# Kernel optimization log

Measured on AMD Instinct MI355X. Metric: run time of the kernel, lower is better.

## Reference

```python
import jax, jax.numpy as jnp
import numpy as np

B, N, W, D, K = 128, 256, 64, 128, 20
EPS_BN = 1e-5   # BatchNorm eps (eval mode, running stats = (0, 1))
ALPHA = 0.7     # cosine vs temporal-correlation mixing weight
SLOPE = 0.2     # LeakyReLU negative slope in attention


def setup_inputs() -> dict:
    key = jax.random.key(0)
    ks = jax.random.split(key, 10)
    return {
        "data": jax.random.normal(ks[0], (B, N, W), jnp.float32),
        "org_edge_index": jax.random.randint(ks[1], (2, 4), 0, N),  # unused by forward
        "emb_weight": jax.random.normal(ks[2], (N, D), jnp.float32) * 0.1,
        "lin_W": jax.random.normal(ks[3], (W, D), jnp.float32) / np.sqrt(W),
        "att_i": jax.random.normal(ks[4], (D,), jnp.float32) * 0.1,
        "att_j": jax.random.normal(ks[5], (D,), jnp.float32) * 0.1,
        "att_em_i": jax.random.normal(ks[6], (D,), jnp.float32) * 0.1,
        "att_em_j": jax.random.normal(ks[7], (D,), jnp.float32) * 0.1,
        "gnn_bias": jnp.zeros((D,), jnp.float32),
        "bn1_gamma": jnp.ones((D,), jnp.float32),
        "bn1_beta": jnp.zeros((D,), jnp.float32),
        "bn2_gamma": jnp.ones((D,), jnp.float32),
        "bn2_beta": jnp.zeros((D,), jnp.float32),
        "out_W": jax.random.normal(ks[8], (D, 1), jnp.float32) / np.sqrt(D),
        "out_b": jnp.zeros((1,), jnp.float32),
    }


def _gdn_forward(data, emb_weight, lin_W, att_i, att_j, att_em_i, att_em_j,
                 gnn_bias, bn1_gamma, bn1_beta, bn2_gamma, bn2_beta, out_W, out_b):
    B_, N_, W_ = data.shape
    data = jax.lax.stop_gradient(data)  # torch: x = data.clone().detach()
    x = data.reshape(B_ * N_, W_)

    # ---- dynamic graph build (embedding is detached here in the original) ----
    wts = jax.lax.stop_gradient(emb_weight)                      # [N, D]
    nrm = jnp.linalg.norm(wts, axis=-1)
    cos = (wts @ wts.T) / (jnp.outer(nrm, nrm) + 1e-8)
    xr = jnp.transpose(data, (1, 0, 2)).reshape(N_, -1)          # [N, B*W]
    xc = xr - xr.mean(axis=1, keepdims=True)
    cov = xc @ xc.T
    std = jnp.sqrt(jnp.diagonal(cov) + 1e-8)
    corr = cov / (jnp.outer(std, std) + 1e-8)
    sim = ALPHA * cos + (1.0 - ALPHA) * corr
    topk_idx = jax.lax.top_k(sim, K)[1]                          # [N, K]; diag==1.0 so self edge included

    # gated edges: source j = topk neighbor, target i = row node; batched with node offsets.
    gated_j = topk_idx.reshape(-1)                               # [N*K]
    gated_i = jnp.repeat(jnp.arange(N_), K)                      # [N*K]
    offs = jnp.arange(B_) * N_
    src = (gated_j[:, None] + offs[None, :]).reshape(-1)         # [N*K*B]
    dst = (gated_i[:, None] + offs[None, :]).reshape(-1)

    # ---- GAT-style attention (GraphLayer, heads=1, concat=False) ----
    xl = x @ lin_W                                               # [B*N, D]
    emb_all = jnp.tile(emb_weight, (B_, 1))                      # [B*N, D]
    # per-node scores (equivalent to cat((x, emb)) . cat((att, att_em)))
    s_i = xl @ att_i + emb_all @ att_em_i
    s_j = xl @ att_j + emb_all @ att_em_j
    alpha = s_i[dst] + s_j[src]                                  # [E]
    alpha = jnp.where(alpha > 0, alpha, SLOPE * alpha)           # leaky_relu
    nseg = B_ * N_
    amax = jax.ops.segment_max(alpha, dst, num_segments=nseg)
    ex = jnp.exp(alpha - amax[dst])
    denom = jax.ops.segment_sum(ex, dst, num_segments=nseg)
    attw = ex / denom[dst]                                       # softmax over each node's in-edges
    out = jax.ops.segment_sum(xl[src] * attw[:, None], dst, num_segments=nseg)
    out = out + gnn_bias

    # GNNLayer: BatchNorm1d (eval: running stats (0,1)) + ReLU
    out = jax.nn.relu(out / jnp.sqrt(1.0 + EPS_BN) * bn1_gamma + bn1_beta)

    # ---- readout ----
    h = out.reshape(B_, N_, -1) * emb_weight[None]               # [B, N, D]
    h = jax.nn.relu(h / jnp.sqrt(1.0 + EPS_BN) * bn2_gamma + bn2_beta)  # bn_outlayer_in (eval)
    # dropout(0.2) is identity in eval mode
    y = h @ out_W + out_b                                        # OutLayer (layer_num=1): Linear(D, 1)
    return y.reshape(-1, N_)                                     # [B, N]


def reference(data, org_edge_index, emb_weight, lin_W, att_i, att_j, att_em_i, att_em_j,
              gnn_bias, bn1_gamma, bn1_beta, bn2_gamma, bn2_beta, out_W, out_b):
    # org_edge_index is accepted but unused, exactly as in the torch forward.
    return _gdn_forward(data, emb_weight, lin_W, att_i, att_j, att_em_i, att_em_j,
                        gnn_bias, bn1_gamma, bn1_beta, bn2_gamma, bn2_beta, out_W, out_b)
```

## Files before the change

### kernel.cpp

```cpp
#include <hip/hip_runtime.h>
#include <math.h>

#define BB 128
#define NN 256
#define WW 64
#define DD 128
#define KK 20
#define LL (BB*WW)
#define NPAIR (NN*(NN+1)/2)

__global__ __launch_bounds__(256) void k_covpre(const float* __restrict__ data,
                                                const float* __restrict__ emb,
                                                const float* __restrict__ att_em_i,
                                                const float* __restrict__ att_em_j,
                                                float* __restrict__ covp,
                                                double* __restrict__ mean,
                                                float* __restrict__ eemi,
                                                float* __restrict__ eemj,
                                                double* __restrict__ nrm2,
                                                int split, int bpc) {
    const int t = threadIdx.x;
    const int ncov = 20 * split;

    if ((int)blockIdx.x >= ncov) {
        const int pb = blockIdx.x - ncov;
        const int lane = t & 63, wid = t >> 6;
        if (pb < NN) {
            int n = pb;
            double s = 0.0;
            for (int c = 0; c < LL / 256; ++c) {
                int l = t + c * 256;
                int b = l >> 6, w = l & 63;
                s += (double)data[(b * NN + n) * WW + w];
            }
            for (int off = 32; off; off >>= 1) s += __shfl_down(s, off);
            __shared__ double redm[4];
            if (lane == 0) redm[wid] = s;
            __syncthreads();
            if (t == 0) mean[n] = (redm[0] + redm[1] + redm[2] + redm[3]) / (double)LL;
        } else {
            int n = (pb - NN) * 2 + (t >> 7);
            int d = t & 127;
            float e = emb[n * DD + d];
            float pi = e * att_em_i[d];
            float pj = e * att_em_j[d];
            double pn = (double)e * (double)e;
            for (int off = 32; off; off >>= 1) {
                pi += __shfl_down(pi, off);
                pj += __shfl_down(pj, off);
                pn += __shfl_down(pn, off);
            }
            __shared__ float ri[4], rj[4];
            __shared__ double rn[4];
            if (lane == 0) { ri[wid] = pi; rj[wid] = pj; rn[wid] = pn; }
            __syncthreads();
            if ((t & 127) == 0) {
                int w0 = (t >> 7) * 2;
                eemi[n] = ri[w0] + ri[w0 + 1];
                eemj[n] = rj[w0] + rj[w0 + 1];
                nrm2[n] = rn[w0] + rn[w0 + 1];
            }
        }
        return;
    }

    const int tile = blockIdx.x % 20;
    const int bz = blockIdx.x / 20;
    int rem = tile, bi = 0;
    while (rem >= 8 - 2 * bi) { rem -= 8 - 2 * bi; ++bi; }
    const int i0 = bi * 64;
    const int j0 = (2 * bi + rem) * 32;

    const int ti = t >> 4, tj = t & 15;

    __shared__ float As[64][68];
    __shared__ float Bs[32][68];

    const int b0 = bz * bpc;
    float acc[4][2] = {};

    #pragma unroll 1
    for (int cb = 0; cb < bpc; ++cb) {
        const int b = b0 + cb;
        #pragma unroll
        for (int e = 0; e < 4; ++e) {
            int idx = t + e * 256, row = idx >> 4, q = idx & 15;
            float4 va = ((const float4*)(data + ((size_t)b * NN + i0 + row) * WW))[q];
            *(float4*)&As[row][4 * q] = va;
        }
        #pragma unroll
        for (int e = 0; e < 2; ++e) {
            int idx = t + e * 256, row = idx >> 4, q = idx & 15;
            float4 vb = ((const float4*)(data + ((size_t)b * NN + j0 + row) * WW))[q];
            *(float4*)&Bs[row][4 * q] = vb;
        }
        __syncthreads();

        #pragma unroll 4
        for (int q = 0; q < 16; ++q) {
            float4 b0v = *(const float4*)&Bs[tj][4 * q];
            float4 b1v = *(const float4*)&Bs[tj + 16][4 * q];
            #pragma unroll
            for (int r = 0; r < 4; ++r) {
                float4 af = *(const float4*)&As[ti + 16 * r][4 * q];
                acc[r][0] += af.x * b0v.x + af.y * b0v.y + af.z * b0v.z + af.w * b0v.w;
                acc[r][1] += af.x * b1v.x + af.y * b1v.y + af.z * b1v.z + af.w * b1v.w;
            }
        }
        __syncthreads();
    }

    #pragma unroll
    for (int r = 0; r < 4; ++r)
        #pragma unroll
        for (int c = 0; c < 2; ++c)
            covp[((size_t)bz * NN + i0 + ti + 16 * r) * NN + j0 + tj + 16 * c] = acc[r][c];
}

__global__ __launch_bounds__(256) void k_phase2(const float* __restrict__ covp,
                                                const double* __restrict__ mean,
                                                double* __restrict__ cov,
                                                const float* __restrict__ data,
                                                const float* __restrict__ linW,
                                                const float* __restrict__ att_i,
                                                const float* __restrict__ att_j,
                                                const float* __restrict__ eemi,
                                                const float* __restrict__ eemj,
                                                float* __restrict__ xl,
                                                float* __restrict__ sil,
                                                float* __restrict__ sjl,
                                                int split) {
    __shared__ float Xs[128][68];
    __shared__ float Wt[DD][68];
    const int t = threadIdx.x;

    if (blockIdx.x >= NN) {
        int idx = (blockIdx.x - NN) * 256 + t;
        if (idx >= NPAIR) return;
        double dn = (double)(2 * NN + 1);
        int i = (int)((dn - sqrt(dn * dn - 8.0 * (double)idx)) * 0.5);
        while ((i + 1) * (2 * NN - i) / 2 <= idx) ++i;
        while (i * (2 * NN - i + 1) / 2 > idx) --i;
        int j = i + (idx - i * (2 * NN - i + 1) / 2);

        double s = 0.0;
        for (int z = 0; z < split; ++z) s += (double)covp[((size_t)z * NN + i) * NN + j];
        s -= (double)LL * mean[i] * mean[j];
        cov[i * NN + j] = s;
        if (i != j) cov[j * NN + i] = s;
        return;
    }

    const int r0 = blockIdx.x * 128;
    const int ti = t >> 4, tj = t & 15;

    #pragma unroll
    for (int e = 0; e < 8; ++e) {
        int idx = t + e * 256, row = idx >> 4, q = idx & 15;
        float4 v = ((const float4*)(data + (size_t)(r0 + row) * WW))[q];
        *(float4*)&Xs[row][4 * q] = v;
    }
    #pragma unroll
    for (int e = 0; e < 32; ++e) {
        int idx = t + e * 256;
        int k = idx >> 7, col = idx & 127;
        Wt[col][k] = linW[idx];
    }
    __syncthreads();

    float acc[8][8] = {};
    #pragma unroll
    for (int q = 0; q < 16; ++q) {
        float4 wb[8];
        #pragma unroll
        for (int c = 0; c < 8; ++c) wb[c] = *(const float4*)&Wt[tj + 16 * c][4 * q];
        #pragma unroll
        for (int r = 0; r < 8; ++r) {
            float4 xa = *(const float4*)&Xs[8 * ti + r][4 * q];
            #pragma unroll
            for (int c = 0; c < 8; ++c)
                acc[r][c] += xa.x * wb[c].x + xa.y * wb[c].y
                           + xa.z * wb[c].z + xa.w * wb[c].w;
        }
    }
    #pragma unroll
    for (int r = 0; r < 8; ++r)
        #pragma unroll
        for (int c = 0; c < 8; ++c)
            xl[(size_t)(r0 + 8 * ti + r) * DD + tj + 16 * c] = acc[r][c];

    float ai[8], aj[8];
    #pragma unroll
    for (int c = 0; c < 8; ++c) { ai[c] = att_i[tj + 16 * c]; aj[c] = att_j[tj + 16 * c]; }
    #pragma unroll
    for (int r = 0; r < 8; ++r) {
        float pi = 0.f, pj = 0.f;
        #pragma unroll
        for (int c = 0; c < 8; ++c) { pi += acc[r][c] * ai[c]; pj += acc[r][c] * aj[c]; }
        #pragma unroll
        for (int m = 8; m; m >>= 1) { pi += __shfl_xor(pi, m); pj += __shfl_xor(pj, m); }
        if (tj == 0) {
            int v = r0 + 8 * ti + r;
            int node = v & (NN - 1);
            sil[v] = pi + eemi[node];
            sjl[v] = pj + eemj[node];
        }
    }
}

__global__ void k_sim_topk(const float* __restrict__ emb,
                           const double* __restrict__ nrm2,
                           const double* __restrict__ cov,
                           int* __restrict__ topk) {
    int i = blockIdx.x;
    int t = threadIdx.x;
    __shared__ float embI[DD];
    __shared__ float sim[NN];

    if (t < DD) embI[t] = emb[i * DD + t];
    __syncthreads();

    const float4* er = (const float4*)(emb + (size_t)t * DD);
    double dot = 0.0;
    #pragma unroll 8
    for (int d4 = 0; d4 < DD / 4; ++d4) {
        float4 v = er[d4];
        dot += (double)embI[4 * d4 + 0] * (double)v.x
             + (double)embI[4 * d4 + 1] * (double)v.y
             + (double)embI[4 * d4 + 2] * (double)v.z
             + (double)embI[4 * d4 + 3] * (double)v.w;
    }
    double cosv = dot / (sqrt(nrm2[i]) * sqrt(nrm2[t]) + 1e-8);
    double stdi = sqrt(cov[i * NN + i] + 1e-8);
    double stdj = sqrt(cov[t * NN + t] + 1e-8);
    double corrv = cov[i * NN + t] / (stdi * stdj + 1e-8);
    sim[t] = (float)(0.7 * cosv + 0.3 * corrv);
    __syncthreads();

    float my = sim[t];
    int cnt = 0;
    #pragma unroll 8
    for (int u = 0; u < NN; ++u) {
        float s = sim[u];
        cnt += (s > my || (s == my && u < t)) ? 1 : 0;
    }
    if (cnt < KK) topk[i * KK + cnt] = t;
}

__global__ __launch_bounds__(512) void k_attn2(
        const float* __restrict__ xl, const int* __restrict__ topk,
        const float* __restrict__ sil, const float* __restrict__ sjl,
        const float* __restrict__ gnn_bias,
        const float* __restrict__ bn1_g, const float* __restrict__ bn1_b,
        const float* __restrict__ bn2_g, const float* __restrict__ bn2_b,
        const float* __restrict__ emb,
        const float* __restrict__ outW, const float* __restrict__ outb,
        float* __restrict__ out) {
    const int h = blockIdx.x;
    const int b = blockIdx.y;
    const int t = threadIdx.x;
    const int lane = t & 63, wv = t >> 6;
    const int q = lane & 31, half = lane >> 5;

    __shared__ float xls[NN * DD];
    __shared__ int2 jwS[128 * KK];

    {
        const float4* src = (const float4*)(xl + (size_t)b * NN * DD);
        float4* dst = (float4*)xls;
        #pragma unroll
        for (int e = 0; e < 16; ++e) dst[t + e * 512] = src[t + e * 512];
    }

    if (t < 128) {
        int i = h * 128 + t;
        float si = sil[b * NN + i];
        int jj[KK]; float aa[KK];
        float amax = -3.4e38f;
        #pragma unroll
        for (int k = 0; k < KK; ++k) {
            int j = topk[i * KK + k];
            jj[k] = j;
            float a = si + sjl[b * NN + j];
            a = a > 0.f ? a : 0.2f * a;
            aa[k] = a;
            amax = fmaxf(amax, a);
        }
        float den = 0.f;
        #pragma unroll
        for (int k = 0; k < KK; ++k) { float e = expf(aa[k] - amax); aa[k] = e; den += e; }
        float r = 1.f / den;
        #pragma unroll
        for (int k = 0; k < KK; ++k)
            jwS[t * KK + k] = make_int2(jj[k], __float_as_int(aa[k] * r));
    }
    __syncthreads();

    const float rbnd = 1.0f / sqrtf(1.0f + 1e-5f);
    const float4 gb = ((const float4*)gnn_bias)[q];
    const float4 g1 = ((const float4*)bn1_g)[q];
    const float4 b1 = ((const float4*)bn1_b)[q];
    const float4 g2 = ((const float4*)bn2_g)[q];
    const float4 b2 = ((const float4*)bn2_b)[q];
    const float4 ow = ((const float4*)outW)[q];
    const float ob0 = outb[0];

    for (int n = 0; n < 8; ++n) {
        int il = wv * 16 + 2 * n + half;
        int i  = h * 128 + il;

        float ax = 0.f, ay = 0.f, az = 0.f, aw = 0.f;
        #pragma unroll
        for (int k = 0; k < KK; ++k) {
            int2 p = jwS[il * KK + k];
            float w = __int_as_float(p.y);
            float4 xv = *(const float4*)&xls[p.x * DD + 4 * q];
            ax += w * xv.x; ay += w * xv.y; az += w * xv.z; aw += w * xv.w;
        }

        float4 em = *(const float4*)&emb[(size_t)i * DD + 4 * q];
        float o0 = (ax + gb.x) * rbnd * g1.x + b1.x; o0 = fmaxf(o0, 0.f);
        float o1 = (ay + gb.y) * rbnd * g1.y + b1.y; o1 = fmaxf(o1, 0.f);
        float o2 = (az + gb.z) * rbnd * g1.z + b1.z; o2 = fmaxf(o2, 0.f);
        float o3 = (aw + gb.w) * rbnd * g1.w + b1.w; o3 = fmaxf(o3, 0.f);
        float h0 = o0 * em.x * rbnd * g2.x + b2.x; h0 = fmaxf(h0, 0.f);
        float h1 = o1 * em.y * rbnd * g2.y + b2.y; h1 = fmaxf(h1, 0.f);
        float h2 = o2 * em.z * rbnd * g2.z + b2.z; h2 = fmaxf(h2, 0.f);
        float h3 = o3 * em.w * rbnd * g2.w + b2.w; h3 = fmaxf(h3, 0.f);

        float p4 = h0 * ow.x + h1 * ow.y + h2 * ow.z + h3 * ow.w;
        #pragma unroll
        for (int off = 16; off; off >>= 1) p4 += __shfl_xor(p4, off);
        if (q == 0) out[b * NN + i] = p4 + ob0;
    }
}

extern "C" void kernel_launch(void* const* d_in, const int* in_sizes, int n_in,
                              void* d_out, int out_size, void* d_ws, size_t ws_size,
                              hipStream_t stream) {
    const float* data     = (const float*)d_in[0];
    const float* emb      = (const float*)d_in[2];
    const float* linW     = (const float*)d_in[3];
    const float* att_i    = (const float*)d_in[4];
    const float* att_j    = (const float*)d_in[5];
    const float* att_em_i = (const float*)d_in[6];
    const float* att_em_j = (const float*)d_in[7];
    const float* gnn_bias = (const float*)d_in[8];
    const float* bn1_g    = (const float*)d_in[9];
    const float* bn1_b    = (const float*)d_in[10];
    const float* bn2_g    = (const float*)d_in[11];
    const float* bn2_b    = (const float*)d_in[12];
    const float* outW     = (const float*)d_in[13];
    const float* outb     = (const float*)d_in[14];
    float* out = (float*)d_out;

    char* ws = (char*)d_ws;
    double* mean  = (double*)(ws + 0);
    double* nrm2  = (double*)(ws + 2048);
    float*  eemi  = (float*)(ws + 4096);
    float*  eemj  = (float*)(ws + 5120);
    int*    topk  = (int*)(ws + 8192);
    double* cov   = (double*)(ws + 32768);
    float*  covp  = (float*)(ws + (1 << 20));
    float*  sil   = (float*)(ws + (30 << 20));
    float*  sjl   = (float*)(ws + (30 << 20) + (128 << 10));
    float*  xl    = (float*)(ws + (32 << 20));

    int split = (ws_size >= (size_t)(48 << 20) + (1 << 20)) ? 64 : 32;
    int bpc = BB / split;

    k_covpre<<<20 * split + NN + NN / 2, 256, 0, stream>>>(
        data, emb, att_em_i, att_em_j, covp, mean, eemi, eemj, nrm2, split, bpc);
    k_phase2<<<NN + (NPAIR + 255) / 256, 256, 0, stream>>>(
        covp, mean, cov, data, linW, att_i, att_j, eemi, eemj, xl, sil, sjl, split);
    k_sim_topk<<<NN, 256, 0, stream>>>(emb, nrm2, cov, topk);
    dim3 ga(2, BB);
    k_attn2<<<ga, 512, 0, stream>>>(xl, topk, sil, sjl, gnn_bias,
                                    bn1_g, bn1_b, bn2_g, bn2_b, emb, outW, outb, out);
}
```

Measured before the change: 72.48 us.

## Merge covariance, projection and stats into one kernel; fold cov reduction into top-k

Folds the covariance partial GEMM, the xl projection with attention scores, and the per-node mean/embedding stats into a single launch. Covariance tiles become three 128x128 upper-triangle tiles with a larger batch split. The split reduction and mean correction move into the top-k kernel, with the diagonal variance computed directly from sums of squares. The embedding attention terms are now added inside the attention kernel. This removes one launch and the separate pair-reduction pass, at the cost of fewer, heavier cov blocks and more covp reads in top-k.

```diff
diff --git a/kernel.cpp b/kernel.cpp
--- a/kernel.cpp
+++ b/kernel.cpp
@@ -7,217 +7,202 @@
 #define DD 128
 #define KK 20
 #define LL (BB*WW)
-#define NPAIR (NN*(NN+1)/2)
-
-__global__ __launch_bounds__(256) void k_covpre(const float* __restrict__ data,
-                                                const float* __restrict__ emb,
-                                                const float* __restrict__ att_em_i,
-                                                const float* __restrict__ att_em_j,
-                                                float* __restrict__ covp,
-                                                double* __restrict__ mean,
-                                                float* __restrict__ eemi,
-                                                float* __restrict__ eemj,
-                                                double* __restrict__ nrm2,
-                                                int split, int bpc) {
+
+__global__ __launch_bounds__(256) void k_mega(const float* __restrict__ data,
+                                              const float* __restrict__ emb,
+                                              const float* __restrict__ linW,
+                                              const float* __restrict__ att_i,
+                                              const float* __restrict__ att_j,
+                                              const float* __restrict__ att_em_i,
+                                              const float* __restrict__ att_em_j,
+                                              float* __restrict__ covp,
+                                              double* __restrict__ mean,
+                                              double* __restrict__ diagc,
+                                              float* __restrict__ eemi,
+                                              float* __restrict__ eemj,
+                                              double* __restrict__ nrm2,
+                                              float* __restrict__ xl,
+                                              float* __restrict__ sil,
+                                              float* __restrict__ sjl,
+                                              int split, int bpc) {
+    __shared__ float As[128][68];
+    __shared__ float Bs[128][68];
     const int t = threadIdx.x;
-    const int ncov = 20 * split;
-
-    if ((int)blockIdx.x >= ncov) {
-        const int pb = blockIdx.x - ncov;
-        const int lane = t & 63, wid = t >> 6;
-        if (pb < NN) {
-            int n = pb;
-            double s = 0.0;
-            for (int c = 0; c < LL / 256; ++c) {
-                int l = t + c * 256;
-                int b = l >> 6, w = l & 63;
-                s += (double)data[(b * NN + n) * WW + w];
+    const int bx = blockIdx.x;
+    const int ncov = 3 * split;
+
+    if (bx < ncov) {
+        const int tile = bx / split, bz = bx % split;
+        const int bi = (tile == 2) ? 1 : 0;
+        const int bj = (tile == 0) ? 0 : 1;
+        const int i0 = bi * 128, j0 = bj * 128;
+        const int ti = t >> 4, tj = t & 15;
+
+        float acc[8][8] = {};
+        const int b0 = bz * bpc;
+
+        #pragma unroll 1
+        for (int cb = 0; cb < bpc; ++cb) {
+            const int b = b0 + cb;
+            #pragma unroll
+            for (int e = 0; e < 8; ++e) {
+                int idx = t + e * 256, row = idx >> 4, q = idx & 15;
+                *(float4*)&As[row][4 * q] =
+                    ((const float4*)(data + ((size_t)b * NN + i0 + row) * WW))[q];
+                *(float4*)&Bs[row][4 * q] =
+                    ((const float4*)(data + ((size_t)b * NN + j0 + row) * WW))[q];
             }
-            for (int off = 32; off; off >>= 1) s += __shfl_down(s, off);
-            __shared__ double redm[4];
-            if (lane == 0) redm[wid] = s;
             __syncthreads();
-            if (t == 0) mean[n] = (redm[0] + redm[1] + redm[2] + redm[3]) / (double)LL;
-        } else {
-            int n = (pb - NN) * 2 + (t >> 7);
-            int d = t & 127;
-            float e = emb[n * DD + d];
-            float pi = e * att_em_i[d];
-            float pj = e * att_em_j[d];
-            double pn = (double)e * (double)e;
-            for (int off = 32; off; off >>= 1) {
-                pi += __shfl_down(pi, off);
-                pj += __shfl_down(pj, off);
-                pn += __shfl_down(pn, off);
+            #pragma unroll
+            for (int q = 0; q < 16; ++q) {
+                float4 wb[8];
+                #pragma unroll
+                for (int c = 0; c < 8; ++c) wb[c] = *(const float4*)&Bs[tj + 16 * c][4 * q];
+                #pragma unroll
+                for (int r = 0; r < 8; ++r) {
+                    float4 xa = *(const float4*)&As[8 * ti + r][4 * q];
+                    #pragma unroll
+                    for (int c = 0; c < 8; ++c)
+                        acc[r][c] += xa.x * wb[c].x + xa.y * wb[c].y
+                                   + xa.z * wb[c].z + xa.w * wb[c].w;
+                }
             }
-            __shared__ float ri[4], rj[4];
-            __shared__ double rn[4];
-            if (lane == 0) { ri[wid] = pi; rj[wid] = pj; rn[wid] = pn; }
             __syncthreads();
-            if ((t & 127) == 0) {
-                int w0 = (t >> 7) * 2;
-                eemi[n] = ri[w0] + ri[w0 + 1];
-                eemj[n] = rj[w0] + rj[w0 + 1];
-                nrm2[n] = rn[w0] + rn[w0 + 1];
+        }
+        #pragma unroll
+        for (int r = 0; r < 8; ++r)
+            #pragma unroll
+            for (int c = 0; c < 8; ++c)
+                covp[((size_t)bz * NN + i0 + 8 * ti + r) * NN + j0 + tj + 16 * c] = acc[r][c];
+        return;
+    }
+
+    if (bx < ncov + 256) {
+        const int r0 = (bx - ncov) * 128;
+        const int ti = t >> 4, tj = t & 15;
+
+        #pragma unroll
+        for (int e = 0; e < 8; ++e) {
+            int idx = t + e * 256, row = idx >> 4, q = idx & 15;
+            *(float4*)&As[row][4 * q] =
+                ((const float4*)(data + (size_t)(r0 + row) * WW))[q];
+        }
+        #pragma unroll
+        for (int e = 0; e < 32; ++e) {
+            int idx = t + e * 256;
+            int k = idx >> 7, col = idx & 127;
+            Bs[col][k] = linW[idx];
+        }
+        __syncthreads();
+
+        float acc[8][8] = {};
+        #pragma unroll
+        for (int q = 0; q < 16; ++q) {
+            float4 wb[8];
+            #pragma unroll
+            for (int c = 0; c < 8; ++c) wb[c] = *(const float4*)&Bs[tj + 16 * c][4 * q];
+            #pragma unroll
+            for (int r = 0; r < 8; ++r) {
+                float4 xa = *(const float4*)&As[8 * ti + r][4 * q];
+                #pragma unroll
+                for (int c = 0; c < 8; ++c)
+                    acc[r][c] += xa.x * wb[c].x + xa.y * wb[c].y
+                               + xa.z * wb[c].z + xa.w * wb[c].w;
             }
         }
+        #pragma unroll
+        for (int r = 0; r < 8; ++r)
+            #pragma unroll
+            for (int c = 0; c < 8; ++c)
+                xl[(size_t)(r0 + 8 * ti + r) * DD + tj + 16 * c] = acc[r][c];
+
+        float ai[8], aj[8];
+        #pragma unroll
+        for (int c = 0; c < 8; ++c) { ai[c] = att_i[tj + 16 * c]; aj[c] = att_j[tj + 16 * c]; }
+        #pragma unroll
+        for (int r = 0; r < 8; ++r) {
+            float pi = 0.f, pj = 0.f;
+            #pragma unroll
+            for (int c = 0; c < 8; ++c) { pi += acc[r][c] * ai[c]; pj += acc[r][c] * aj[c]; }
+            #pragma unroll
+            for (int m = 8; m; m >>= 1) { pi += __shfl_xor(pi, m); pj += __shfl_xor(pj, m); }
+            if (tj == 0) {
+                int v = r0 + 8 * ti + r;
+                sil[v] = pi;
+                sjl[v] = pj;
+            }
+        }
         return;
     }
 
-    const int tile = blockIdx.x % 20;
-    const int bz = blockIdx.x / 20;
-    int rem = tile, bi = 0;
-    while (rem >= 8 - 2 * bi) { rem -= 8 - 2 * bi; ++bi; }
-    const int i0 = bi * 64;
-    const int j0 = (2 * bi + rem) * 32;
-
-    const int ti = t >> 4, tj = t & 15;
-
-    __shared__ float As[64][68];
-    __shared__ float Bs[32][68];
-
-    const int b0 = bz * bpc;
-    float acc[4][2] = {};
-
-    #pragma unroll 1
-    for (int cb = 0; cb < bpc; ++cb) {
-        const int b = b0 + cb;
-        #pragma unroll
-        for (int e = 0; e < 4; ++e) {
-            int idx = t + e * 256, row = idx >> 4, q = idx & 15;
-            float4 va = ((const float4*)(data + ((size_t)b * NN + i0 + row) * WW))[q];
-            *(float4*)&As[row][4 * q] = va;
-        }
-        #pragma unroll
-        for (int e = 0; e < 2; ++e) {
-            int idx = t + e * 256, row = idx >> 4, q = idx & 15;
-            float4 vb = ((const float4*)(data + ((size_t)b * NN + j0 + row) * WW))[q];
-            *(float4*)&Bs[row][4 * q] = vb;
-        }
+    const int pb = bx - ncov - 256;
+    const int lane = t & 63, wid = t >> 6;
+    if (pb < NN) {
+        int n = pb;
+        double s = 0.0, s2 = 0.0;
+        for (int c = 0; c < LL / 256; ++c) {
+            int l = t + c * 256;
+            int b = l >> 6, w = l & 63;
+            double v = (double)data[(b * NN + n) * WW + w];
+            s += v; s2 += v * v;
+        }
+        for (int off = 32; off; off >>= 1) {
+            s += __shfl_down(s, off);
+            s2 += __shfl_down(s2, off);
+        }
+        __shared__ double redm[4], redq[4];
+        if (lane == 0) { redm[wid] = s; redq[wid] = s2; }
         __syncthreads();
-
-        #pragma unroll 4
-        for (int q = 0; q < 16; ++q) {
-            float4 b0v = *(const float4*)&Bs[tj][4 * q];
-            float4 b1v = *(const float4*)&Bs[tj + 16][4 * q];
-            #pragma unroll
-            for (int r = 0; r < 4; ++r) {
-                float4 af = *(const float4*)&As[ti + 16 * r][4 * q];
-                acc[r][0] += af.x * b0v.x + af.y * b0v.y + af.z * b0v.z + af.w * b0v.w;
-                acc[r][1] += af.x * b1v.x + af.y * b1v.y + af.z * b1v.z + af.w * b1v.w;
-            }
-        }
+        if (t == 0) {
+            double S = redm[0] + redm[1] + redm[2] + redm[3];
+            double S2 = redq[0] + redq[1] + redq[2] + redq[3];
+            double m = S / (double)LL;
+            mean[n] = m;
+            diagc[n] = S2 - (double)LL * m * m;
+        }
+    } else {
+        int n = (pb - NN) * 2 + (t >> 7);
+        int d = t & 127;
+        float e = emb[n * DD + d];
+        float pi = e * att_em_i[d];
+        float pj = e * att_em_j[d];
+        double pn = (double)e * (double)e;
+        for (int off = 32; off; off >>= 1) {
+            pi += __shfl_down(pi, off);
+            pj += __shfl_down(pj, off);
+            pn += __shfl_down(pn, off);
+        }
+        __shared__ float ri[4], rj[4];
+        __shared__ double rn[4];
+        if (lane == 0) { ri[wid] = pi; rj[wid] = pj; rn[wid] = pn; }
         __syncthreads();
-    }
-
-    #pragma unroll
-    for (int r = 0; r < 4; ++r)
-        #pragma unroll
-        for (int c = 0; c < 2; ++c)
-            covp[((size_t)bz * NN + i0 + ti + 16 * r) * NN + j0 + tj + 16 * c] = acc[r][c];
+        if ((t & 127) == 0) {
+            int w0 = (t >> 7) * 2;
+            eemi[n] = ri[w0] + ri[w0 + 1];
+            eemj[n] = rj[w0] + rj[w0 + 1];
+            nrm2[n] = rn[w0] + rn[w0 + 1];
+        }
+    }
 }
 
-__global__ __launch_bounds__(256) void k_phase2(const float* __restrict__ covp,
-                                                const double* __restrict__ mean,
-                                                double* __restrict__ cov,
-                                                const float* __restrict__ data,
-                                                const float* __restrict__ linW,
-                                                const float* __restrict__ att_i,
-                                                const float* __restrict__ att_j,
-                                                const float* __restrict__ eemi,
-                                                const float* __restrict__ eemj,
-                                                float* __restrict__ xl,
-                                                float* __restrict__ sil,
-                                                float* __restrict__ sjl,
-                                                int split) {
-    __shared__ float Xs[128][68];
-    __shared__ float Wt[DD][68];
-    const int t = threadIdx.x;
-
-    if (blockIdx.x >= NN) {
-        int idx = (blockIdx.x - NN) * 256 + t;
-        if (idx >= NPAIR) return;
-        double dn = (double)(2 * NN + 1);
-        int i = (int)((dn - sqrt(dn * dn - 8.0 * (double)idx)) * 0.5);
-        while ((i + 1) * (2 * NN - i) / 2 <= idx) ++i;
-        while (i * (2 * NN - i + 1) / 2 > idx) --i;
-        int j = i + (idx - i * (2 * NN - i + 1) / 2);
-
-        double s = 0.0;
-        for (int z = 0; z < split; ++z) s += (double)covp[((size_t)z * NN + i) * NN + j];
-        s -= (double)LL * mean[i] * mean[j];
-        cov[i * NN + j] = s;
-        if (i != j) cov[j * NN + i] = s;
-        return;
-    }
-
-    const int r0 = blockIdx.x * 128;
-    const int ti = t >> 4, tj = t & 15;
-
-    #pragma unroll
-    for (int e = 0; e < 8; ++e) {
-        int idx = t + e * 256, row = idx >> 4, q = idx & 15;
-        float4 v = ((const float4*)(data + (size_t)(r0 + row) * WW))[q];
-        *(float4*)&Xs[row][4 * q] = v;
-    }
-    #pragma unroll
-    for (int e = 0; e < 32; ++e) {
-        int idx = t + e * 256;
-        int k = idx >> 7, col = idx & 127;
-        Wt[col][k] = linW[idx];
-    }
-    __syncthreads();
-
-    float acc[8][8] = {};
-    #pragma unroll
-    for (int q = 0; q < 16; ++q) {
-        float4 wb[8];
-        #pragma unroll
-        for (int c = 0; c < 8; ++c) wb[c] = *(const float4*)&Wt[tj + 16 * c][4 * q];
-        #pragma unroll
-        for (int r = 0; r < 8; ++r) {
-            float4 xa = *(const float4*)&Xs[8 * ti + r][4 * q];
-            #pragma unroll
-            for (int c = 0; c < 8; ++c)
-                acc[r][c] += xa.x * wb[c].x + xa.y * wb[c].y
-                           + xa.z * wb[c].z + xa.w * wb[c].w;
-        }
-    }
-    #pragma unroll
-    for (int r = 0; r < 8; ++r)
-        #pragma unroll
-        for (int c = 0; c < 8; ++c)
-            xl[(size_t)(r0 + 8 * ti + r) * DD + tj + 16 * c] = acc[r][c];
-
-    float ai[8], aj[8];
-    #pragma unroll
-    for (int c = 0; c < 8; ++c) { ai[c] = att_i[tj + 16 * c]; aj[c] = att_j[tj + 16 * c]; }
-    #pragma unroll
-    for (int r = 0; r < 8; ++r) {
-        float pi = 0.f, pj = 0.f;
-        #pragma unroll
-        for (int c = 0; c < 8; ++c) { pi += acc[r][c] * ai[c]; pj += acc[r][c] * aj[c]; }
-        #pragma unroll
-        for (int m = 8; m; m >>= 1) { pi += __shfl_xor(pi, m); pj += __shfl_xor(pj, m); }
-        if (tj == 0) {
-            int v = r0 + 8 * ti + r;
-            int node = v & (NN - 1);
-            sil[v] = pi + eemi[node];
-            sjl[v] = pj + eemj[node];
-        }
-    }
-}
-
-__global__ void k_sim_topk(const float* __restrict__ emb,
+__global__ void k_simtopk2(const float* __restrict__ covp,
+                           const double* __restrict__ mean,
+                           const double* __restrict__ diagc,
+                           const float* __restrict__ emb,
                            const double* __restrict__ nrm2,
-                           const double* __restrict__ cov,
-                           int* __restrict__ topk) {
+                           int* __restrict__ topk, int split) {
     int i = blockIdx.x;
     int t = threadIdx.x;
     __shared__ float embI[DD];
     __shared__ float sim[NN];
 
     if (t < DD) embI[t] = emb[i * DD + t];
+
+    size_t base = (i < 128 || t >= 128) ? ((size_t)i * NN + t) : ((size_t)t * NN + i);
+    double s = 0.0;
+    for (int z = 0; z < split; ++z) s += (double)covp[(size_t)z * NN * NN + base];
+    s -= (double)LL * mean[i] * mean[t];
+
     __syncthreads();
 
     const float4* er = (const float4*)(emb + (size_t)t * DD);
@@ -231,9 +216,9 @@
              + (double)embI[4 * d4 + 3] * (double)v.w;
     }
     double cosv = dot / (sqrt(nrm2[i]) * sqrt(nrm2[t]) + 1e-8);
-    double stdi = sqrt(cov[i * NN + i] + 1e-8);
-    double stdj = sqrt(cov[t * NN + t] + 1e-8);
-    double corrv = cov[i * NN + t] / (stdi * stdj + 1e-8);
+    double stdi = sqrt(diagc[i] + 1e-8);
+    double stdj = sqrt(diagc[t] + 1e-8);
+    double corrv = s / (stdi * stdj + 1e-8);
     sim[t] = (float)(0.7 * cosv + 0.3 * corrv);
     __syncthreads();
 
@@ -241,15 +226,16 @@
     int cnt = 0;
     #pragma unroll 8
     for (int u = 0; u < NN; ++u) {
-        float s = sim[u];
-        cnt += (s > my || (s == my && u < t)) ? 1 : 0;
+        float sv = sim[u];
+        cnt += (sv > my || (sv == my && u < t)) ? 1 : 0;
     }
     if (cnt < KK) topk[i * KK + cnt] = t;
 }
 
-__global__ __launch_bounds__(512) void k_attn2(
+__global__ __launch_bounds__(512) void k_attn3(
         const float* __restrict__ xl, const int* __restrict__ topk,
         const float* __restrict__ sil, const float* __restrict__ sjl,
+        const float* __restrict__ eemi, const float* __restrict__ eemj,
         const float* __restrict__ gnn_bias,
         const float* __restrict__ bn1_g, const float* __restrict__ bn1_b,
         const float* __restrict__ bn2_g, const float* __restrict__ bn2_b,
@@ -274,14 +260,14 @@
 
     if (t < 128) {
         int i = h * 128 + t;
-        float si = sil[b * NN + i];
+        float si = sil[b * NN + i] + eemi[i];
         int jj[KK]; float aa[KK];
         float amax = -3.4e38f;
         #pragma unroll
         for (int k = 0; k < KK; ++k) {
             int j = topk[i * KK + k];
             jj[k] = j;
-            float a = si + sjl[b * NN + j];
+            float a = si + sjl[b * NN + j] + eemj[j];
             a = a > 0.f ? a : 0.2f * a;
             aa[k] = a;
             amax = fmaxf(amax, a);
@@ -359,22 +345,21 @@
     double* nrm2  = (double*)(ws + 2048);
     float*  eemi  = (float*)(ws + 4096);
     float*  eemj  = (float*)(ws + 5120);
+    double* diagc = (double*)(ws + 6144);
     int*    topk  = (int*)(ws + 8192);
-    double* cov   = (double*)(ws + 32768);
+    float*  sil   = (float*)(ws + (64 << 10));
+    float*  sjl   = (float*)(ws + (192 << 10));
     float*  covp  = (float*)(ws + (1 << 20));
-    float*  sil   = (float*)(ws + (30 << 20));
-    float*  sjl   = (float*)(ws + (30 << 20) + (128 << 10));
-    float*  xl    = (float*)(ws + (32 << 20));
-
-    int split = (ws_size >= (size_t)(48 << 20) + (1 << 20)) ? 64 : 32;
+    float*  xl    = (float*)(ws + (36 << 20));
+
+    int split = (ws_size >= (size_t)(53 << 20)) ? 128 : 64;
     int bpc = BB / split;
 
-    k_covpre<<<20 * split + NN + NN / 2, 256, 0, stream>>>(
-        data, emb, att_em_i, att_em_j, covp, mean, eemi, eemj, nrm2, split, bpc);
-    k_phase2<<<NN + (NPAIR + 255) / 256, 256, 0, stream>>>(
-        covp, mean, cov, data, linW, att_i, att_j, eemi, eemj, xl, sil, sjl, split);
-    k_sim_topk<<<NN, 256, 0, stream>>>(emb, nrm2, cov, topk);
+    k_mega<<<3 * split + 256 + 256 + 128, 256, 0, stream>>>(
+        data, emb, linW, att_i, att_j, att_em_i, att_em_j,
+        covp, mean, diagc, eemi, eemj, nrm2, xl, sil, sjl, split, bpc);
+    k_simtopk2<<<NN, 256, 0, stream>>>(covp, mean, diagc, emb, nrm2, topk, split);
     dim3 ga(2, BB);
-    k_attn2<<<ga, 512, 0, stream>>>(xl, topk, sil, sjl, gnn_bias,
+    k_attn3<<<ga, 512, 0, stream>>>(xl, topk, sil, sjl, eemi, eemj, gnn_bias,
                                     bn1_g, bn1_b, bn2_g, bn2_b, emb, outW, outb, out);
 }
```

Measured after the change: 146.1 us. 102% more time.

## Use square 64x64 covariance tiles with larger batch split and unrolled partial reduction

Applied to the files above, without the earlier changes.

The covariance Gram kernel switches from 64x32 tiles (20 per split) to 64x64 upper-triangular tiles (10 per split). Each thread now accumulates a 4x4 block, which raises reuse of the shared-memory loads, and the batch split doubles to 64 or 128 partials to keep enough blocks in flight. The partial-sum reduction in phase2 now uses 8 independent double accumulators to expose memory-level parallelism. The topk kernel issues its covariance loads before the barrier. The cost is more partial-sum traffic and more register pressure, and the reduction loop assumes split is a multiple of 8.

```diff
diff --git a/kernel.cpp b/kernel.cpp
--- a/kernel.cpp
+++ b/kernel.cpp
@@ -19,113 +19,110 @@
                                                 float* __restrict__ eemj,
                                                 double* __restrict__ nrm2,
                                                 int split, int bpc) {
+    __shared__ float As[64][68];
+    __shared__ float Bs[64][68];
     const int t = threadIdx.x;
-    const int ncov = 20 * split;
-
-    if ((int)blockIdx.x >= ncov) {
-        const int pb = blockIdx.x - ncov;
-        const int lane = t & 63, wid = t >> 6;
-        if (pb < NN) {
-            int n = pb;
-            double s = 0.0;
-            for (int c = 0; c < LL / 256; ++c) {
-                int l = t + c * 256;
-                int b = l >> 6, w = l & 63;
-                s += (double)data[(b * NN + n) * WW + w];
+    const int bx = blockIdx.x;
+    const int ncov = 10 * split;
+
+    if (bx < ncov) {
+        const int tile = bx % 10, bz = bx / 10;
+        int rem = tile, bi = 0;
+        while (rem >= 4 - bi) { rem -= 4 - bi; ++bi; }
+        const int i0 = bi * 64;
+        const int j0 = (bi + rem) * 64;
+        const int ti = t >> 4, tj = t & 15;
+
+        float acc[4][4] = {};
+        const int b0 = bz * bpc;
+
+        #pragma unroll 1
+        for (int cb = 0; cb < bpc; ++cb) {
+            const int b = b0 + cb;
+            #pragma unroll
+            for (int e = 0; e < 4; ++e) {
+                int idx = t + e * 256, row = idx >> 4, q = idx & 15;
+                *(float4*)&As[row][4 * q] =
+                    ((const float4*)(data + ((size_t)b * NN + i0 + row) * WW))[q];
+                *(float4*)&Bs[row][4 * q] =
+                    ((const float4*)(data + ((size_t)b * NN + j0 + row) * WW))[q];
             }
-            for (int off = 32; off; off >>= 1) s += __shfl_down(s, off);
-            __shared__ double redm[4];
-            if (lane == 0) redm[wid] = s;
             __syncthreads();
-            if (t == 0) mean[n] = (redm[0] + redm[1] + redm[2] + redm[3]) / (double)LL;
-        } else {
-            int n = (pb - NN) * 2 + (t >> 7);
-            int d = t & 127;
-            float e = emb[n * DD + d];
-            float pi = e * att_em_i[d];
-            float pj = e * att_em_j[d];
-            double pn = (double)e * (double)e;
-            for (int off = 32; off; off >>= 1) {
-                pi += __shfl_down(pi, off);
-                pj += __shfl_down(pj, off);
-                pn += __shfl_down(pn, off);
+
+            #pragma unroll 4
+            for (int q = 0; q < 16; ++q) {
+                float4 wb[4];
+                #pragma unroll
+                for (int c = 0; c < 4; ++c) wb[c] = *(const float4*)&Bs[tj + 16 * c][4 * q];
+                #pragma unroll
+                for (int r = 0; r < 4; ++r) {
+                    float4 xa = *(const float4*)&As[ti + 16 * r][4 * q];
+                    #pragma unroll
+                    for (int c = 0; c < 4; ++c)
+                        acc[r][c] += xa.x * wb[c].x + xa.y * wb[c].y
+                                   + xa.z * wb[c].z + xa.w * wb[c].w;
+                }
             }
-            __shared__ float ri[4], rj[4];
-            __shared__ double rn[4];
-            if (lane == 0) { ri[wid] = pi; rj[wid] = pj; rn[wid] = pn; }
             __syncthreads();
-            if ((t & 127) == 0) {
-                int w0 = (t >> 7) * 2;
-                eemi[n] = ri[w0] + ri[w0 + 1];
-                eemj[n] = rj[w0] + rj[w0 + 1];
-                nrm2[n] = rn[w0] + rn[w0 + 1];
-            }
-        }
+        }
+
+        #pragma unroll
+        for (int r = 0; r < 4; ++r)
+            #pragma unroll
+            for (int c = 0; c < 4; ++c)
+                covp[((size_t)bz * NN + i0 + ti + 16 * r) * NN + j0 + tj + 16 * c] = acc[r][c];
         return;
     }
 
-    const int tile = blockIdx.x % 20;
-    const int bz = blockIdx.x / 20;
-    int rem = tile, bi = 0;
-    while (rem >= 8 - 2 * bi) { rem -= 8 - 2 * bi; ++bi; }
-    const int i0 = bi * 64;
-    const int j0 = (2 * bi + rem) * 32;
-
-    const int ti = t >> 4, tj = t & 15;
-
-    __shared__ float As[64][68];
-    __shared__ float Bs[32][68];
-
-    const int b0 = bz * bpc;
-    float acc[4][2] = {};
-
-    #pragma unroll 1
-    for (int cb = 0; cb < bpc; ++cb) {
-        const int b = b0 + cb;
-        #pragma unroll
-        for (int e = 0; e < 4; ++e) {
-            int idx = t + e * 256, row = idx >> 4, q = idx & 15;
-            float4 va = ((const float4*)(data + ((size_t)b * NN + i0 + row) * WW))[q];
-            *(float4*)&As[row][4 * q] = va;
-        }
-        #pragma unroll
-        for (int e = 0; e < 2; ++e) {
-            int idx = t + e * 256, row = idx >> 4, q = idx & 15;
-            float4 vb = ((const float4*)(data + ((size_t)b * NN + j0 + row) * WW))[q];
-            *(float4*)&Bs[row][4 * q] = vb;
-        }
+    const int pb = bx - ncov;
+    const int lane = t & 63, wid = t >> 6;
+    if (pb < NN) {
+        int n = pb;
+        double s = 0.0;
+        for (int c = 0; c < LL / 256; ++c) {
+            int l = t + c * 256;
+            int b = l >> 6, w = l & 63;
+            s += (double)data[(b * NN + n) * WW + w];
+        }
+        for (int off = 32; off; off >>= 1) s += __shfl_down(s, off);
+        __shared__ double redm[4];
+        if (lane == 0) redm[wid] = s;
         __syncthreads();
-
-        #pragma unroll 4
-        for (int q = 0; q < 16; ++q) {
-            float4 b0v = *(const float4*)&Bs[tj][4 * q];
-            float4 b1v = *(const float4*)&Bs[tj + 16][4 * q];
-            #pragma unroll
-            for (int r = 0; r < 4; ++r) {
-                float4 af = *(const float4*)&As[ti + 16 * r][4 * q];
-                acc[r][0] += af.x * b0v.x + af.y * b0v.y + af.z * b0v.z + af.w * b0v.w;
-                acc[r][1] += af.x * b1v.x + af.y * b1v.y + af.z * b1v.z + af.w * b1v.w;
-            }
-        }
+        if (t == 0) mean[n] = (redm[0] + redm[1] + redm[2] + redm[3]) / (double)LL;
+    } else {
+        int n = (pb - NN) * 2 + (t >> 7);
+        int d = t & 127;
+        float e = emb[n * DD + d];
+        float pi = e * att_em_i[d];
+        float pj = e * att_em_j[d];
+        double pn = (double)e * (double)e;
+        for (int off = 32; off; off >>= 1) {
+            pi += __shfl_down(pi, off);
+            pj += __shfl_down(pj, off);
+            pn += __shfl_down(pn, off);
+        }
+        __shared__ float ri[4], rj[4];
+        __shared__ double rn[4];
+        if (lane == 0) { ri[wid] = pi; rj[wid] = pj; rn[wid] = pn; }
         __syncthreads();
-    }
-
-    #pragma unroll
-    for (int r = 0; r < 4; ++r)
-        #pragma unroll
-        for (int c = 0; c < 2; ++c)
-            covp[((size_t)bz * NN + i0 + ti + 16 * r) * NN + j0 + tj + 16 * c] = acc[r][c];
-}
-
-__global__ __launch_bounds__(256) void k_phase2(const float* __restrict__ covp,
-                                                const double* __restrict__ mean,
-                                                double* __restrict__ cov,
-                                                const float* __restrict__ data,
+        if ((t & 127) == 0) {
+            int w0 = (t >> 7) * 2;
+            eemi[n] = ri[w0] + ri[w0 + 1];
+            eemj[n] = rj[w0] + rj[w0 + 1];
+            nrm2[n] = rn[w0] + rn[w0 + 1];
+        }
+    }
+}
+
+__global__ __launch_bounds__(256) void k_phase2(const float* __restrict__ data,
                                                 const float* __restrict__ linW,
                                                 const float* __restrict__ att_i,
                                                 const float* __restrict__ att_j,
                                                 const float* __restrict__ eemi,
                                                 const float* __restrict__ eemj,
+                                                const float* __restrict__ covp,
+                                                const double* __restrict__ mean,
+                                                double* __restrict__ cov,
                                                 float* __restrict__ xl,
                                                 float* __restrict__ sil,
                                                 float* __restrict__ sjl,
@@ -133,9 +130,10 @@
     __shared__ float Xs[128][68];
     __shared__ float Wt[DD][68];
     const int t = threadIdx.x;
-
-    if (blockIdx.x >= NN) {
-        int idx = (blockIdx.x - NN) * 256 + t;
+    const int bx = blockIdx.x;
+
+    if (bx >= NN) {
+        int idx = (bx - NN) * 256 + t;
         if (idx >= NPAIR) return;
         double dn = (double)(2 * NN + 1);
         int i = (int)((dn - sqrt(dn * dn - 8.0 * (double)idx)) * 0.5);
@@ -143,22 +141,35 @@
         while (i * (2 * NN - i + 1) / 2 > idx) --i;
         int j = i + (idx - i * (2 * NN - i + 1) / 2);
 
-        double s = 0.0;
-        for (int z = 0; z < split; ++z) s += (double)covp[((size_t)z * NN + i) * NN + j];
+        const float* p = covp + (size_t)i * NN + j;
+        const size_t NS = (size_t)NN * NN;
+        double s0 = 0, s1 = 0, s2 = 0, s3 = 0, s4 = 0, s5 = 0, s6 = 0, s7 = 0;
+        for (int z = 0; z < split; z += 8) {
+            const float* qz = p + (size_t)z * NS;
+            s0 += (double)qz[0];
+            s1 += (double)qz[NS];
+            s2 += (double)qz[2 * NS];
+            s3 += (double)qz[3 * NS];
+            s4 += (double)qz[4 * NS];
+            s5 += (double)qz[5 * NS];
+            s6 += (double)qz[6 * NS];
+            s7 += (double)qz[7 * NS];
+        }
+        double s = ((s0 + s1) + (s2 + s3)) + ((s4 + s5) + (s6 + s7));
         s -= (double)LL * mean[i] * mean[j];
-        cov[i * NN + j] = s;
-        if (i != j) cov[j * NN + i] = s;
+        cov[(size_t)i * NN + j] = s;
+        if (i != j) cov[(size_t)j * NN + i] = s;
         return;
     }
 
-    const int r0 = blockIdx.x * 128;
+    const int r0 = bx * 128;
     const int ti = t >> 4, tj = t & 15;
 
     #pragma unroll
     for (int e = 0; e < 8; ++e) {
         int idx = t + e * 256, row = idx >> 4, q = idx & 15;
-        float4 v = ((const float4*)(data + (size_t)(r0 + row) * WW))[q];
-        *(float4*)&Xs[row][4 * q] = v;
+        *(float4*)&Xs[row][4 * q] =
+            ((const float4*)(data + (size_t)(r0 + row) * WW))[q];
     }
     #pragma unroll
     for (int e = 0; e < 32; ++e) {
@@ -208,9 +219,9 @@
     }
 }
 
-__global__ void k_sim_topk(const float* __restrict__ emb,
+__global__ void k_simtopk3(const double* __restrict__ cov,
+                           const float* __restrict__ emb,
                            const double* __restrict__ nrm2,
-                           const double* __restrict__ cov,
                            int* __restrict__ topk) {
     int i = blockIdx.x;
     int t = threadIdx.x;
@@ -218,6 +229,9 @@
     __shared__ float sim[NN];
 
     if (t < DD) embI[t] = emb[i * DD + t];
+    double s = cov[(size_t)i * NN + t];
+    double stdi = sqrt(cov[(size_t)i * NN + i] + 1e-8);
+    double stdj = sqrt(cov[(size_t)t * NN + t] + 1e-8);
     __syncthreads();
 
     const float4* er = (const float4*)(emb + (size_t)t * DD);
@@ -231,9 +245,7 @@
              + (double)embI[4 * d4 + 3] * (double)v.w;
     }
     double cosv = dot / (sqrt(nrm2[i]) * sqrt(nrm2[t]) + 1e-8);
-    double stdi = sqrt(cov[i * NN + i] + 1e-8);
-    double stdj = sqrt(cov[t * NN + t] + 1e-8);
-    double corrv = cov[i * NN + t] / (stdi * stdj + 1e-8);
+    double corrv = s / (stdi * stdj + 1e-8);
     sim[t] = (float)(0.7 * cosv + 0.3 * corrv);
     __syncthreads();
 
@@ -241,8 +253,8 @@
     int cnt = 0;
     #pragma unroll 8
     for (int u = 0; u < NN; ++u) {
-        float s = sim[u];
-        cnt += (s > my || (s == my && u < t)) ? 1 : 0;
+        float sv = sim[u];
+        cnt += (sv > my || (sv == my && u < t)) ? 1 : 0;
     }
     if (cnt < KK) topk[i * KK + cnt] = t;
 }
@@ -355,25 +367,25 @@
     float* out = (float*)d_out;
 
     char* ws = (char*)d_ws;
-    double* mean  = (double*)(ws + 0);
-    double* nrm2  = (double*)(ws + 2048);
-    float*  eemi  = (float*)(ws + 4096);
-    float*  eemj  = (float*)(ws + 5120);
-    int*    topk  = (int*)(ws + 8192);
-    double* cov   = (double*)(ws + 32768);
-    float*  covp  = (float*)(ws + (1 << 20));
-    float*  sil   = (float*)(ws + (30 << 20));
-    float*  sjl   = (float*)(ws + (30 << 20) + (128 << 10));
-    float*  xl    = (float*)(ws + (32 << 20));
-
-    int split = (ws_size >= (size_t)(48 << 20) + (1 << 20)) ? 64 : 32;
+    double* mean   = (double*)(ws + 0);
+    double* nrm2   = (double*)(ws + 2048);
+    float*  eemi   = (float*)(ws + 4096);
+    float*  eemj   = (float*)(ws + 5120);
+    int*    topk   = (int*)(ws + 8192);
+    float*  sil    = (float*)(ws + (64 << 10));
+    float*  sjl    = (float*)(ws + (192 << 10));
+    double* cov    = (double*)(ws + (320 << 10));
+    float*  covp   = (float*)(ws + (1 << 20));
+    float*  xl     = (float*)(ws + (36 << 20));
+
+    int split = (ws_size >= (size_t)(53 << 20)) ? 128 : 64;
     int bpc = BB / split;
 
-    k_covpre<<<20 * split + NN + NN / 2, 256, 0, stream>>>(
+    k_covpre<<<10 * split + NN + NN / 2, 256, 0, stream>>>(
         data, emb, att_em_i, att_em_j, covp, mean, eemi, eemj, nrm2, split, bpc);
     k_phase2<<<NN + (NPAIR + 255) / 256, 256, 0, stream>>>(
-        covp, mean, cov, data, linW, att_i, att_j, eemi, eemj, xl, sil, sjl, split);
-    k_sim_topk<<<NN, 256, 0, stream>>>(emb, nrm2, cov, topk);
+        data, linW, att_i, att_j, eemi, eemj, covp, mean, cov, xl, sil, sjl, split);
+    k_simtopk3<<<NN, 256, 0, stream>>>(cov, emb, nrm2, topk);
     dim3 ga(2, BB);
     k_attn2<<<ga, 512, 0, stream>>>(xl, topk, sil, sjl, gnn_bias,
                                     bn1_g, bn1_b, bn2_g, bn2_b, emb, outW, outb, out);
```

After: 68.72 us, median of 2. 5.2% less time.
